# Kernel optimization log

Measured on AMD Instinct MI355X. Metric: run time of the kernel, lower is better.

The kernel has to match this reference:

```python
import jax, jax.numpy as jnp
import numpy as np

N_HEAD = 16


def _rope(x, cos, sin):
    # x: [B, T, H, hd]; cos/sin: [1, T, 1, hd//2] (interleaved-pair rotation)
    x1, x2 = x[..., ::2], x[..., 1::2]
    r1 = x1 * cos - x2 * sin
    r2 = x1 * sin + x2 * cos
    return jnp.stack([r1, r2], axis=-1).reshape(x.shape)


def setup_inputs() -> dict:
    key = jax.random.key(0)
    k1, k2, k3 = jax.random.split(key, 3)
    B, T, D = 2, 2048, 2048
    x = jax.random.normal(k1, (B, T, D), dtype=jnp.float32)
    w_attn = jax.random.normal(k2, (3 * D, D), dtype=jnp.float32) * 0.02
    w_proj = jax.random.normal(k3, (D, D), dtype=jnp.float32) * 0.02
    return {"x": x, "w_attn": w_attn, "w_proj": w_proj}


def reference(x, w_attn, w_proj):
    B, T, D = x.shape
    H = N_HEAD
    hd = D // H
    # fused QKV projection (bias=False)
    qkv = x @ w_attn.T                      # [B, T, 3D]
    q, k, v = jnp.split(qkv, 3, axis=-1)
    q = q.reshape(B, T, H, hd)
    k = k.reshape(B, T, H, hd)
    v = v.reshape(B, T, H, hd)
    # RoPE tables: inv_freq = 1/10000^(2i/hd), angles m*theta_i
    inv_freq = 1.0 / (10000.0 ** (jnp.arange(0, hd, 2, dtype=jnp.float32) / hd))
    t = jnp.arange(T, dtype=jnp.float32)
    freqs = t[:, None] * inv_freq[None, :]  # [T, hd//2]
    cos = jnp.cos(freqs)[None, :, None, :]
    sin = jnp.sin(freqs)[None, :, None, :]
    q = _rope(q, cos, sin)
    k = _rope(k, cos, sin)
    # causal attention with materialized [B,H,T,T] scores (as in source)
    scale = 1.0 / np.sqrt(hd).astype(np.float32)
    att = jnp.einsum('bthd,bshd->bhts', q, k) * scale
    causal = jnp.tril(jnp.ones((T, T), dtype=bool))
    att = jnp.where(causal, att, -jnp.inf)
    att = jax.nn.softmax(att, axis=-1)
    y = jnp.einsum('bhts,bshd->bthd', att, v).reshape(B, T, D)
    return y @ w_proj.T
```

## Files before the change

kernel.cpp:

```cpp
#include <hip/hip_runtime.h>
#include <hip/hip_bf16.h>

#define T_SEQ 2048
#define DMODEL 2048
#define NB 2
#define NH 16
#define HD 128
#define BK 64

typedef __attribute__((ext_vector_type(8))) short short8;
typedef __attribute__((ext_vector_type(4))) float f32x4;
typedef __attribute__((ext_vector_type(16))) float f32x16;
typedef unsigned short ushort_t;

__device__ inline ushort_t f2bf(float f) {
  union { float f; unsigned u; } v; v.f = f;
  unsigned r = v.u + 0x7fffu + ((v.u >> 16) & 1u);
  return (ushort_t)(r >> 16);
}
__device__ inline float bf2f(ushort_t u) {
  union { unsigned u; float f; } v; v.u = ((unsigned)u) << 16;
  return v.f;
}
__device__ inline unsigned pk2(float x, float y) {
  union { __hip_bfloat162 h; unsigned u; } c;
  c.h = __float22bfloat162_rn(float2{x, y});
  return c.u;
}
__device__ inline float fexp2(float x) {
  float r;
  asm("v_exp_f32 %0, %1" : "=v"(r) : "v"(x));
  return r;
}

__device__ inline void gload16(const void* g, void* l) {
  __builtin_amdgcn_global_load_lds(
      (const __attribute__((address_space(1))) unsigned*)g,
      (__attribute__((address_space(3))) unsigned*)l, 16, 0, 0);
}

__global__ void cvt_f32_bf16(const float* __restrict__ src, ushort_t* __restrict__ dst, int n8) {
  int i = blockIdx.x * blockDim.x + threadIdx.x;
  if (i >= n8) return;
  const float4* s = (const float4*)src + (size_t)i * 2;
  float4 a = s[0], b = s[1];
  short8 o;
  o[0] = (short)f2bf(a.x); o[1] = (short)f2bf(a.y);
  o[2] = (short)f2bf(a.z); o[3] = (short)f2bf(a.w);
  o[4] = (short)f2bf(b.x); o[5] = (short)f2bf(b.y);
  o[6] = (short)f2bf(b.z); o[7] = (short)f2bf(b.w);
  *((short8*)dst + i) = o;
}

__global__ void trig_init(float* __restrict__ trig) {
  int idx = blockIdx.x * blockDim.x + threadIdx.x;
  if (idx >= T_SEQ * 64) return;
  int i = idx & 63, t = idx >> 6;
  float inv = __expf(-(float)i * (9.210340371976184f / 64.0f));
  float f = (float)t * inv;
  trig[idx * 2]     = cosf(f);
  trig[idx * 2 + 1] = sinf(f);
}

__global__ __launch_bounds__(256)
void v_transpose(const ushort_t* __restrict__ v, ushort_t* __restrict__ vt) {
  __shared__ __align__(16) ushort_t L[64][136];
  int bh = blockIdx.y;
  int t0 = blockIdx.x * 64;
  int tid = threadIdx.x;
  int row = tid >> 2, c0 = (tid & 3) * 32;
  const ushort_t* src = v + ((size_t)bh * T_SEQ + t0 + row) * HD + c0;
#pragma unroll
  for (int j = 0; j < 4; ++j)
    *(short8*)&L[row][c0 + j * 8] = *(const short8*)(src + j * 8);
  __syncthreads();
  int d = tid >> 1, tc = (tid & 1) * 32;
  union { ushort_t u[32]; short8 v8[4]; } buf;
#pragma unroll
  for (int j = 0; j < 32; ++j) buf.u[j] = L[tc + j][d];
  ushort_t* dst = vt + ((size_t)bh * HD + d) * T_SEQ + t0 + tc;
#pragma unroll
  for (int j = 0; j < 4; ++j) *(short8*)(dst + j * 8) = buf.v8[j];
}

template <int EPI>
__global__ __launch_bounds__(512, 2)
void gemm256(const ushort_t* __restrict__ A, const ushort_t* __restrict__ Bt,
             float* __restrict__ C, ushort_t* __restrict__ q_t,
             ushort_t* __restrict__ k_t, ushort_t* __restrict__ v_t,
             const float* __restrict__ trig, int M, int N, int K) {
  __shared__ __align__(16) ushort_t sA[2][256 * 64];
  __shared__ __align__(16) ushort_t sB[2][256 * 64];
  int tid = threadIdx.x, lane = tid & 63, w = tid >> 6;
  int wm = w >> 2, wn = w & 3;
  int li = lane & 15, lg = lane >> 4;
  int tile_m = blockIdx.y * 256, tile_n = blockIdx.x * 256;
  const ushort_t* Ag = A + (size_t)tile_m * K;
  const ushort_t* Bg = Bt + (size_t)tile_n * K;

  int srow = w * 16 + (lane >> 3);
  int schunk = ((lane & 7) ^ (lane >> 3)) * 8;

  auto stageA = [&](int half, int kt, int buf) {
#pragma unroll
    for (int i = 0; i < 2; ++i) {
      int row = half * 128 + srow + i * 8;
      gload16(Ag + (size_t)row * K + kt * BK + schunk,
              &sA[buf][half * 8192 + w * 1024 + i * 512]);
    }
  };
  auto stageB = [&](int half, int kt, int buf) {
#pragma unroll
    for (int i = 0; i < 2; ++i) {
      int row = half * 128 + srow + i * 8;
      gload16(Bg + (size_t)row * K + kt * BK + schunk,
              &sB[buf][half * 8192 + w * 1024 + i * 512]);
    }
  };

  f32x4 acc[8][4] = {};
  short8 bfr[4][2];
  const int NT = K / BK;

  stageA(0, 0, 0); stageA(1, 0, 0); stageB(0, 0, 0); stageB(1, 0, 0);
  asm volatile("s_waitcnt vmcnt(0)" ::: "memory");
  __syncthreads();

  for (int kt = 0; kt < NT; ++kt) {
    int cur = kt & 1;
    bool pref = (kt + 1 < NT);
#pragma unroll
    for (int p = 0; p < 4; ++p) {
      short8 af[2][2];
#pragma unroll
      for (int mm = 0; mm < 2; ++mm) {
        int row = wm * 128 + (p * 2 + mm) * 16 + li;
#pragma unroll
        for (int kh = 0; kh < 2; ++kh)
          af[mm][kh] = *(const short8*)&sA[cur][row * 64 + (((kh * 4 + lg) ^ (row & 7)) * 8)];
      }
      if (p == 0) {
#pragma unroll
        for (int n = 0; n < 4; ++n) {
          int row = wn * 64 + n * 16 + li;
#pragma unroll
          for (int kh = 0; kh < 2; ++kh)
            bfr[n][kh] = *(const short8*)&sB[cur][row * 64 + (((kh * 4 + lg) ^ (row & 7)) * 8)];
        }
      }
      if (pref) {
        if (p == 0) { stageA(0, kt + 1, cur ^ 1); stageB(0, kt + 1, cur ^ 1); }
        else if (p == 1) { stageA(1, kt + 1, cur ^ 1); stageB(1, kt + 1, cur ^ 1); }
      }
      __builtin_amdgcn_s_barrier();
      asm volatile("s_waitcnt lgkmcnt(0)" ::: "memory");
      __builtin_amdgcn_sched_barrier(0);
      __builtin_amdgcn_s_setprio(1);
#pragma unroll
      for (int mm = 0; mm < 2; ++mm)
#pragma unroll
        for (int n = 0; n < 4; ++n)
#pragma unroll
          for (int kh = 0; kh < 2; ++kh)
            acc[p * 2 + mm][n] = __builtin_amdgcn_mfma_f32_16x16x32_bf16(
                af[mm][kh], bfr[n][kh], acc[p * 2 + mm][n], 0, 0, 0);
      __builtin_amdgcn_s_setprio(0);
      if (p == 3) asm volatile("s_waitcnt vmcnt(0)" ::: "memory");
      __builtin_amdgcn_s_barrier();
    }
  }

  if (EPI == 0) {
#pragma unroll
    for (int m = 0; m < 8; ++m) {
      int trow = tile_m + wm * 128 + m * 16 + lg * 4;
#pragma unroll
      for (int n = 0; n < 4; ++n) {
        int col = tile_n + wn * 64 + n * 16 + li;
#pragma unroll
        for (int r = 0; r < 4; ++r)
          C[(size_t)(trow + r) * N + col] = acc[m][n][r];
      }
    }
  } else {
    int sec = tile_n >> 11;
    int bq  = tile_m >> 11;
    int t0  = tile_m & 2047;
#pragma unroll
    for (int m = 0; m < 8; ++m) {
      int tl = wm * 128 + m * 16 + lg * 4;
#pragma unroll
      for (int n = 0; n < 4; ++n) {
        int nn = (tile_n & 2047) + wn * 64 + n * 16 + li;
        int h = nn >> 7, d = nn & 127;
        if (sec < 2) {
          ushort_t* base = ((sec == 0) ? q_t : k_t) + ((size_t)(bq * NH + h)) * T_SEQ * HD;
          int fi2 = (d >> 1) * 2;
#pragma unroll
          for (int r = 0; r < 4; ++r) {
            int t = t0 + tl + r;
            float val = acc[m][n][r];
            float par = __shfl_xor(val, 1);
            const float* tp = trig + t * 128 + fi2;
            float c = tp[0], s = tp[1];
            float outv = (li & 1) ? (par * s + val * c) : (val * c - par * s);
            base[(size_t)t * HD + d] = f2bf(outv);
          }
        } else {
          ushort_t* base = v_t + ((size_t)(bq * NH + h)) * T_SEQ * HD;
#pragma unroll
          for (int r = 0; r < 4; ++r)
            base[(size_t)(t0 + tl + r) * HD + d] = f2bf(acc[m][n][r]);
        }
      }
    }
  }
}

__global__ __launch_bounds__(256, 2)
void flash_attn(const ushort_t* __restrict__ Q, const ushort_t* __restrict__ Kg,
                const ushort_t* __restrict__ Vt, ushort_t* __restrict__ Y) {
  __shared__ __align__(16) ushort_t ldsK[2 * 64 * 128];
  __shared__ __align__(16) ushort_t ldsV[2 * 128 * 64];
  int tid = threadIdx.x, lane = tid & 63, w = tid >> 6;
  int hi = lane >> 5, l31 = lane & 31;
  int qi = (blockIdx.y & 16) ? (15 - (int)blockIdx.x) : (int)blockIdx.x;
  int bh = blockIdx.y;
  int b = bh >> 4, h = bh & 15;
  int q0 = qi * 128;
  const ushort_t* Qp = Q + (size_t)bh * T_SEQ * HD;
  const ushort_t* Kp = Kg + (size_t)bh * T_SEQ * HD;
  const ushort_t* Vp = Vt + (size_t)bh * HD * T_SEQ;

  int qg = q0 + w * 32 + l31;
  int qmaxw = q0 + w * 32 + 31;

  auto stage = [&](int kv0, int bsel) {
    ushort_t* Kb = ldsK + bsel * 8192;
    ushort_t* Vb = ldsV + bsel * 8192;
#pragma unroll
    for (int p = 0; p < 4; ++p) {
      int c = p * 256 + w * 64 + lane;
      {
        int row = c >> 4, cc = c & 15;
        int sc = cc ^ (row & 15);
        gload16(Kp + (size_t)(kv0 + row) * HD + sc * 8, Kb + (p * 256 + w * 64) * 8);
      }
      {
        int d = c >> 3, cc = c & 7;
        int sc = cc ^ (d & 7);
        gload16(Vp + (size_t)d * T_SEQ + kv0 + sc * 8, Vb + (p * 256 + w * 64) * 8);
      }
    }
  };

  short8 qf[8];
#pragma unroll
  for (int ds = 0; ds < 8; ++ds)
    qf[ds] = *(const short8*)(Qp + (size_t)qg * HD + ds * 16 + hi * 8);

  f32x16 o[4] = {};
  float mu = -1e30f, l = 0.f;
  const float SIG = 0.12751879523209784f;

  int nkt = 2 * qi + 2;
  stage(0, 0);
  __syncthreads();
  int cur = 0;
  for (int kt = 0; kt < nkt; ++kt) {
    int kv0 = kt * 64;
    if (kt + 1 < nkt) stage((kt + 1) * 64, cur ^ 1);
    if (kv0 <= qmaxw) {
      const ushort_t* Kb = ldsK + cur * 8192;
      const ushort_t* Vb = ldsV + cur * 8192;
      f32x16 sa = {}, sb = {};
      __builtin_amdgcn_s_setprio(1);
#pragma unroll
      for (int ds = 0; ds < 8; ++ds) {
        int cc = ds * 2 + hi;
        short8 k0 = *(const short8*)&Kb[l31 * 128 + ((cc ^ (l31 & 15)) * 8)];
        short8 k1 = *(const short8*)&Kb[(32 + l31) * 128 + ((cc ^ (l31 & 15)) * 8)];
        sa = __builtin_amdgcn_mfma_f32_32x32x16_bf16(k0, qf[ds], sa, 0, 0, 0);
        sb = __builtin_amdgcn_mfma_f32_32x32x16_bf16(k1, qf[ds], sb, 0, 0, 0);
      }
      __builtin_amdgcn_s_setprio(0);
      float p[32];
#pragma unroll
      for (int r = 0; r < 16; ++r) { p[r] = sa[r] * SIG; p[16 + r] = sb[r] * SIG; }
      if (kv0 + 63 > q0 + w * 32) {
#pragma unroll
        for (int r = 0; r < 16; ++r) {
          int loc = (r & 3) + 8 * (r >> 2) + 4 * hi;
          if (kv0 + loc > qg)      p[r]      = -3e38f;
          if (kv0 + 32 + loc > qg) p[16 + r] = -3e38f;
        }
      }
      float tm[16];
#pragma unroll
      for (int i = 0; i < 16; ++i) tm[i] = fmaxf(p[i], p[i + 16]);
#pragma unroll
      for (int st = 8; st >= 1; st >>= 1)
#pragma unroll
        for (int i = 0; i < 8; ++i)
          if (i < st) tm[i] = fmaxf(tm[i], tm[i + st]);
      float pmax = fmaxf(tm[0], __shfl_xor(tm[0], 32));
      bool resc = !__all(pmax <= mu + 11.0f);
      if (resc) {
        float munew = fmaxf(mu, pmax);
        float alpha = fexp2(mu - munew);
        mu = munew;
        l *= alpha;
#pragma unroll
        for (int dsub = 0; dsub < 4; ++dsub)
#pragma unroll
          for (int r = 0; r < 16; ++r) o[dsub][r] *= alpha;
      }
#pragma unroll
      for (int i = 0; i < 32; ++i) p[i] = fexp2(p[i] - mu);
      float ts[16];
#pragma unroll
      for (int i = 0; i < 16; ++i) ts[i] = p[i] + p[i + 16];
#pragma unroll
      for (int st = 8; st >= 1; st >>= 1)
#pragma unroll
        for (int i = 0; i < 8; ++i)
          if (i < st) ts[i] += ts[i + st];
      l += ts[0] + __shfl_xor(ts[0], 32);
      __builtin_amdgcn_s_setprio(1);
#pragma unroll
      for (int s = 0; s < 4; ++s) {
        int rb = (s >> 1) * 16 + (s & 1) * 8;
        unsigned a0 = pk2(p[rb + 0], p[rb + 1]);
        unsigned a1 = pk2(p[rb + 2], p[rb + 3]);
        unsigned a2 = pk2(p[rb + 4], p[rb + 5]);
        unsigned a3 = pk2(p[rb + 6], p[rb + 7]);
        unsigned sa0 = (unsigned)__shfl_xor((int)a0, 32);
        unsigned sa1 = (unsigned)__shfl_xor((int)a1, 32);
        unsigned sa2 = (unsigned)__shfl_xor((int)a2, 32);
        unsigned sa3 = (unsigned)__shfl_xor((int)a3, 32);
        union { unsigned u[4]; short8 s8; } pf;
        pf.u[0] = hi ? sa2 : a0;
        pf.u[1] = hi ? sa3 : a1;
        pf.u[2] = hi ? a2 : sa0;
        pf.u[3] = hi ? a3 : sa1;
#pragma unroll
        for (int dsub = 0; dsub < 4; ++dsub) {
          int row = dsub * 32 + l31;
          short8 vf = *(const short8*)&Vb[row * 64 + (((2 * s + hi) ^ (row & 7)) * 8)];
          o[dsub] = __builtin_amdgcn_mfma_f32_32x32x16_bf16(vf, pf.s8, o[dsub], 0, 0, 0);
        }
      }
      __builtin_amdgcn_s_setprio(0);
    }
    __syncthreads();
    cur ^= 1;
  }
  float invl = 1.f / l;
#pragma unroll
  for (int dsub = 0; dsub < 4; ++dsub)
#pragma unroll
    for (int r = 0; r < 16; ++r) o[dsub][r] *= invl;
#pragma unroll
  for (int dsub = 0; dsub < 4; ++dsub)
#pragma unroll
    for (int r = 0; r < 16; r += 2) {
      int d0 = dsub * 32 + (r & 3) + 8 * (r >> 2) + 4 * hi;
      unsigned u = pk2(o[dsub][r], o[dsub][r + 1]);
      *(unsigned*)&ldsK[w * 4096 + l31 * 128 + (((d0 >> 3) ^ (l31 & 15)) * 8) + (d0 & 7)] = u;
    }
  __syncthreads();
#pragma unroll
  for (int rep = 0; rep < 8; ++rep) {
    int idx = rep * 256 + tid;
    int qg2 = idx >> 4, c = idx & 15;
    int wv2 = qg2 >> 5, ql = qg2 & 31;
    short8 val = *(const short8*)&ldsK[wv2 * 4096 + ql * 128 + ((c ^ (ql & 15)) * 8)];
    *(short8*)(Y + ((size_t)(b * T_SEQ + q0 + qg2)) * DMODEL + h * HD + c * 8) = val;
  }
}

extern "C" void kernel_launch(void* const* d_in, const int* in_sizes, int n_in,
                              void* d_out, int out_size, void* d_ws, size_t ws_size,
                              hipStream_t stream) {
  const float* x      = (const float*)d_in[0];
  const float* w_attn = (const float*)d_in[1];
  const float* w_proj = (const float*)d_in[2];
  float* out = (float*)d_out;

  char* ws = (char*)d_ws;
  size_t off = 0;
  auto alloc = [&](size_t bytes) -> void* {
    void* p = ws + off;
    off = (off + bytes + 255) & ~(size_t)255;
    return p;
  };
  const size_t MT = (size_t)NB * T_SEQ;
  ushort_t* xb   = (ushort_t*)alloc(MT * DMODEL * 2);
  ushort_t* wab  = (ushort_t*)alloc((size_t)3 * DMODEL * DMODEL * 2);
  ushort_t* wpb  = (ushort_t*)alloc((size_t)DMODEL * DMODEL * 2);
  ushort_t* q_t  = (ushort_t*)alloc(MT * DMODEL * 2);
  ushort_t* k_t  = (ushort_t*)alloc(MT * DMODEL * 2);
  ushort_t* v_t  = (ushort_t*)alloc(MT * DMODEL * 2);
  ushort_t* vtb  = (ushort_t*)alloc(MT * DMODEL * 2);
  ushort_t* yb   = (ushort_t*)alloc(MT * DMODEL * 2);
  float*    trig = (float*)alloc((size_t)T_SEQ * 64 * 2 * 4);
  (void)ws_size; (void)n_in; (void)in_sizes; (void)out_size;

  {
    int n8x = (int)(MT * DMODEL / 8);
    hipLaunchKernelGGL(cvt_f32_bf16, dim3((n8x + 255) / 256), dim3(256), 0, stream, x, xb, n8x);
    int n8a = (int)((size_t)3 * DMODEL * DMODEL / 8);
    hipLaunchKernelGGL(cvt_f32_bf16, dim3((n8a + 255) / 256), dim3(256), 0, stream, w_attn, wab, n8a);
    int n8p = (int)((size_t)DMODEL * DMODEL / 8);
    hipLaunchKernelGGL(cvt_f32_bf16, dim3((n8p + 255) / 256), dim3(256), 0, stream, w_proj, wpb, n8p);
  }
  hipLaunchKernelGGL(trig_init, dim3(T_SEQ * 64 / 256), dim3(256), 0, stream, trig);

  hipLaunchKernelGGL((gemm256<1>), dim3(3 * DMODEL / 256, MT / 256), dim3(512), 0, stream,
                     xb, wab, (float*)nullptr, q_t, k_t, v_t, trig,
                     (int)MT, 3 * DMODEL, DMODEL);

  hipLaunchKernelGGL(v_transpose, dim3(T_SEQ / 64, NB * NH), dim3(256), 0, stream, v_t, vtb);

  hipLaunchKernelGGL(flash_attn, dim3(T_SEQ / 128, NB * NH), dim3(256), 0, stream,
                     q_t, k_t, vtb, yb);

  hipLaunchKernelGGL((gemm256<0>), dim3(DMODEL / 256, MT / 256), dim3(512), 0, stream,
                     yb, wpb, out, (ushort_t*)nullptr, (ushort_t*)nullptr, (ushort_t*)nullptr,
                     (const float*)nullptr, (int)MT, DMODEL, DMODEL);
}
```

Baseline: 300.4 us.

## Deepen GEMM load pipeline with staggered A/B staging and XCD-aware block swizzle

```diff
diff --git a/kernel.cpp b/kernel.cpp
--- a/kernel.cpp
+++ b/kernel.cpp
@@ -94,7 +94,12 @@
   int tid = threadIdx.x, lane = tid & 63, w = tid >> 6;
   int wm = w >> 2, wn = w & 3;
   int li = lane & 15, lg = lane >> 4;
-  int tile_m = blockIdx.y * 256, tile_n = blockIdx.x * 256;
+  int nwg = gridDim.x * gridDim.y;
+  int flat = blockIdx.y * gridDim.x + blockIdx.x;
+  int cpx = nwg >> 3;
+  int swz = (flat & 7) * cpx + (flat >> 3);
+  int bx = swz % gridDim.x, by = swz / gridDim.x;
+  int tile_m = by * 256, tile_n = bx * 256;
   const ushort_t* Ag = A + (size_t)tile_m * K;
   const ushort_t* Bg = Bt + (size_t)tile_n * K;
 
@@ -120,38 +125,45 @@
 
   f32x4 acc[8][4] = {};
   short8 bfr[4][2];
-  const int NT = K / BK;
-
-  stageA(0, 0, 0); stageA(1, 0, 0); stageB(0, 0, 0); stageB(1, 0, 0);
+  const int NITER = K / (2 * BK);
+
+  stageA(0, 0, 0); stageA(1, 0, 0);
+  stageB(0, 0, 0); stageB(1, 0, 0);
+  stageB(0, 1, 1); stageB(1, 1, 1);
   asm volatile("s_waitcnt vmcnt(0)" ::: "memory");
   __syncthreads();
 
-  for (int kt = 0; kt < NT; ++kt) {
-    int cur = kt & 1;
-    bool pref = (kt + 1 < NT);
-#pragma unroll
-    for (int p = 0; p < 4; ++p) {
+  for (int it = 0; it < NITER; ++it) {
+    int u = 2 * it;
+    bool last = (it == NITER - 1);
+#pragma unroll
+    for (int p = 0; p < 8; ++p) {
+      const int lp = p & 3, buf = p >> 2;
       short8 af[2][2];
 #pragma unroll
       for (int mm = 0; mm < 2; ++mm) {
-        int row = wm * 128 + (p * 2 + mm) * 16 + li;
+        int row = wm * 128 + (lp * 2 + mm) * 16 + li;
 #pragma unroll
         for (int kh = 0; kh < 2; ++kh)
-          af[mm][kh] = *(const short8*)&sA[cur][row * 64 + (((kh * 4 + lg) ^ (row & 7)) * 8)];
-      }
-      if (p == 0) {
+          af[mm][kh] = *(const short8*)&sA[buf][row * 64 + (((kh * 4 + lg) ^ (row & 7)) * 8)];
+      }
+      if (lp == 0) {
 #pragma unroll
         for (int n = 0; n < 4; ++n) {
           int row = wn * 64 + n * 16 + li;
 #pragma unroll
           for (int kh = 0; kh < 2; ++kh)
-            bfr[n][kh] = *(const short8*)&sB[cur][row * 64 + (((kh * 4 + lg) ^ (row & 7)) * 8)];
+            bfr[n][kh] = *(const short8*)&sB[buf][row * 64 + (((kh * 4 + lg) ^ (row & 7)) * 8)];
         }
       }
-      if (pref) {
-        if (p == 0) { stageA(0, kt + 1, cur ^ 1); stageB(0, kt + 1, cur ^ 1); }
-        else if (p == 1) { stageA(1, kt + 1, cur ^ 1); stageB(1, kt + 1, cur ^ 1); }
-      }
+      if (p == 0) stageA(0, u + 1, 1);
+      else if (p == 1) stageA(1, u + 1, 1);
+      else if (p == 2) { if (!last) stageB(0, u + 2, 0); }
+      else if (p == 3) { if (!last) stageB(1, u + 2, 0); }
+      else if (p == 4) { if (!last) stageA(0, u + 2, 0); }
+      else if (p == 5) { if (!last) stageA(1, u + 2, 0); }
+      else if (p == 6) { if (!last) stageB(0, u + 3, 1); }
+      else if (p == 7) { if (!last) stageB(1, u + 3, 1); }
       __builtin_amdgcn_s_barrier();
       asm volatile("s_waitcnt lgkmcnt(0)" ::: "memory");
       __builtin_amdgcn_sched_barrier(0);
@@ -162,10 +174,15 @@
         for (int n = 0; n < 4; ++n)
 #pragma unroll
           for (int kh = 0; kh < 2; ++kh)
-            acc[p * 2 + mm][n] = __builtin_amdgcn_mfma_f32_16x16x32_bf16(
-                af[mm][kh], bfr[n][kh], acc[p * 2 + mm][n], 0, 0, 0);
+            acc[lp * 2 + mm][n] = __builtin_amdgcn_mfma_f32_16x16x32_bf16(
+                af[mm][kh], bfr[n][kh], acc[lp * 2 + mm][n], 0, 0, 0);
       __builtin_amdgcn_s_setprio(0);
-      if (p == 3) asm volatile("s_waitcnt vmcnt(0)" ::: "memory");
+      if (p == 3) {
+        if (last) asm volatile("s_waitcnt vmcnt(0)" ::: "memory");
+        else      asm volatile("s_waitcnt vmcnt(4)" ::: "memory");
+      } else if (p == 7) {
+        if (!last) asm volatile("s_waitcnt vmcnt(4)" ::: "memory");
+      }
       __builtin_amdgcn_s_barrier();
     }
   }
```

New measurement: 327.0 us. +8.9%, slower.
